# Kernel tuning notes

Hardware: AMD Instinct MI355X
Metric: run time of the kernel (lower is better)

Reference implementation:

```python
import jax, jax.numpy as jnp
import numpy as np


def conv2d(x, w, stride=1, padding=0):
    # x: [N,Ci,H,W], w: [Co,Ci,Kh,Kw]
    return jax.lax.conv_general_dilated(
        x, w, window_strides=(stride, stride),
        padding=[(padding, padding), (padding, padding)],
        dimension_numbers=('NCHW', 'OIHW', 'NCHW'))


def adder2d(x, w, stride=1, padding=0):
    """AdderNet L1-distance conv: out[n,co,ho,wo] = -sum_{ci,kh,kw} |x_patch - w[co,ci,kh,kw]|."""
    N, Ci, H, W = x.shape
    Co, _, K, _ = w.shape
    xp = jnp.pad(x, ((0, 0), (0, 0), (padding, padding), (padding, padding)))
    Ho = (H + 2 * padding - K) // stride + 1
    Wo = (W + 2 * padding - K) // stride + 1
    acc = jnp.zeros((N, Co, Ho, Wo), x.dtype)
    for kh in range(K):  # small fixed loop over kernel taps (<=9)
        for kw in range(K):
            xs = xp[:, :, kh:kh + Ho * stride:stride, kw:kw + Wo * stride:stride]  # [N,Ci,Ho,Wo]
            diff = jnp.abs(xs[:, None] - w[None, :, :, kh, kw, None, None])  # [N,Co,Ci,Ho,Wo]
            acc = acc - diff.sum(axis=2)
    return acc


def batchnorm(x, gamma, beta, mean, var, eps=1e-5):
    inv = gamma / jnp.sqrt(var + eps)
    return x * inv[None, :, None, None] + (beta - mean * inv)[None, :, None, None]


def setup_inputs() -> dict:
    key = jax.random.key(0)
    ks = jax.random.split(key, 16)
    N, C, H, W = 4, 128, 28, 28
    inp = {
        'x': jax.random.normal(ks[0], (N, C, H, W), jnp.float32),
        'w_shift1': jax.random.normal(ks[1], (C, C, 1, 1), jnp.float32) * 0.1,
        'w_add1': jax.random.normal(ks[2], (C, C, 1, 1), jnp.float32) * 0.1,
        'bn1_gamma': jax.random.uniform(ks[3], (C,), jnp.float32, 0.5, 1.5),
        'bn1_beta': jax.random.normal(ks[4], (C,), jnp.float32) * 0.1,
        'bn1_mean': jax.random.normal(ks[5], (C,), jnp.float32),
        'bn1_var': jax.random.uniform(ks[6], (C,), jnp.float32, 0.5, 1.5),
        'w_shift2': jax.random.normal(ks[7], (C, C, 3, 3), jnp.float32) * 0.05,
        'w_add2': jax.random.normal(ks[8], (C, C, 3, 3), jnp.float32) * 0.05,
        'bn2_gamma': jax.random.uniform(ks[9], (C,), jnp.float32, 0.5, 1.5),
        'bn2_beta': jax.random.normal(ks[10], (C,), jnp.float32) * 0.1,
        'bn2_mean': jax.random.normal(ks[11], (C,), jnp.float32),
        'bn2_var': jax.random.uniform(ks[12], (C,), jnp.float32, 0.5, 1.5),
    }
    return inp


def reference(x, w_shift1, w_add1, bn1_gamma, bn1_beta, bn1_mean, bn1_var,
              w_shift2, w_add2, bn2_gamma, bn2_beta, bn2_mean, bn2_var):
    identity = x
    # conv1: 1x1 shift conv -> 1x1 adder
    out = conv2d(x, w_shift1, stride=1, padding=0)
    out = adder2d(out, w_add1, stride=1, padding=0)
    out = jax.nn.relu(batchnorm(out, bn1_gamma, bn1_beta, bn1_mean, bn1_var))
    # conv2: 3x3 shift conv (stride=1, pad=1) -> 3x3 adder (stride=1, pad=1)
    out = conv2d(out, w_shift2, stride=1, padding=1)
    out = adder2d(out, w_add2, stride=1, padding=1)
    out = jax.nn.relu(batchnorm(out, bn2_gamma, bn2_beta, bn2_mean, bn2_var))
    return jax.nn.relu(out + identity)
```

## Files before the change

kernel.cpp:

```cpp
#include <hip/hip_runtime.h>
#include <math.h>

constexpr int C   = 128;
constexpr int HW  = 784;
constexpr int PW  = 30;
constexpr int PHW = 900;

#define ABS_ACC(acc, d) asm("v_add_f32 %0, %0, abs(%1)" : "+v"(acc) : "v"(d))

__device__ inline void tile_map2(int wg, int& n, int& h0, int& w0) {
    int region = wg & 7;
    int idx    = wg >> 3;
    n = region >> 1;
    int half = region & 1;
    int th = half * 7 + idx / 14;
    int tw = idx % 14;
    h0 = th * 2;
    w0 = tw * 2;
}

__device__ inline void tile_map4(int wg, int& n, int& h0, int& w0, int& co0) {
    int region = wg & 7;
    int rest   = wg >> 3;
    n = region >> 1;
    int half = region & 1;
    co0 = (rest & 1) * 64;
    int idx = rest >> 1;
    int th = idx / 7, tw = idx % 7;
    h0 = half * 14 + th * 2;
    w0 = tw * 4;
}

__device__ inline void zero_border2(float* plane, int h0, int w0) {
    if (h0 == 0) {
        plane[w0 + 1] = 0.f; plane[w0 + 2] = 0.f;
        if (w0 == 0)  plane[0]  = 0.f;
        if (w0 == 26) plane[29] = 0.f;
    }
    if (h0 == 26) {
        plane[29 * PW + w0 + 1] = 0.f; plane[29 * PW + w0 + 2] = 0.f;
        if (w0 == 0)  plane[29 * PW]      = 0.f;
        if (w0 == 26) plane[29 * PW + 29] = 0.f;
    }
    if (w0 == 0)  { plane[(h0 + 1) * PW]      = 0.f; plane[(h0 + 2) * PW]      = 0.f; }
    if (w0 == 26) { plane[(h0 + 1) * PW + 29] = 0.f; plane[(h0 + 2) * PW + 29] = 0.f; }
}

__device__ inline void zero_border4(float* plane, int h0, int w0) {
    if (h0 == 0) {
#pragma unroll
        for (int c = 0; c < 4; ++c) plane[w0 + 1 + c] = 0.f;
        if (w0 == 0)  plane[0]  = 0.f;
        if (w0 == 24) plane[29] = 0.f;
    }
    if (h0 == 26) {
#pragma unroll
        for (int c = 0; c < 4; ++c) plane[29 * PW + w0 + 1 + c] = 0.f;
        if (w0 == 0)  plane[29 * PW]      = 0.f;
        if (w0 == 24) plane[29 * PW + 29] = 0.f;
    }
    if (w0 == 0)  { plane[(h0 + 1) * PW]      = 0.f; plane[(h0 + 2) * PW]      = 0.f; }
    if (w0 == 24) { plane[(h0 + 1) * PW + 29] = 0.f; plane[(h0 + 2) * PW + 29] = 0.f; }
}

__global__ __launch_bounds__(256) void reorder_w(const float* __restrict__ w2,
                                                 const float* __restrict__ a2,
                                                 const float* __restrict__ w1,
                                                 const float* __restrict__ a1,
                                                 float* __restrict__ w2r,
                                                 float* __restrict__ a2r,
                                                 float* __restrict__ w1r,
                                                 float* __restrict__ a1r) {
    int idx = blockIdx.x * 256 + threadIdx.x;
    const int T9 = C * C * 9;
    const int T1 = C * C;
    if (idx < 2 * T9) {
        const float* src = w2; float* dst = w2r;
        if (idx >= T9) { idx -= T9; src = a2; dst = a2r; }
        int co = idx & 127;
        int r  = idx >> 7;
        int k  = r % 9;
        int ci = r / 9;
        dst[idx] = src[(co * C + ci) * 9 + k];
        return;
    }
    idx -= 2 * T9;
    if (idx >= 2 * T1) return;
    const float* src = w1; float* dst = w1r;
    if (idx >= T1) { idx -= T1; src = a1; dst = a1r; }
    int co = idx & 127;
    int ci = idx >> 7;
    dst[idx] = src[co * C + ci];
}

__global__ __launch_bounds__(256, 8) void stage1(const float* __restrict__ x,
                                                 const float* __restrict__ w1r,
                                                 const float* __restrict__ a1r,
                                                 const float* __restrict__ g1,
                                                 const float* __restrict__ b1,
                                                 const float* __restrict__ m1,
                                                 const float* __restrict__ v1,
                                                 float* __restrict__ t1p) {
    __shared__ float Xs[C][4];
    __shared__ float Ys[C][4];
    __shared__ float Rs[C][4];
    int n, h0, w0;
    tile_map2(blockIdx.x, n, h0, w0);
    int t   = threadIdx.x;
    int co  = t & 127;
    int ciq = t >> 7;
    int ci0 = ciq * 64;

#pragma unroll
    for (int e = t; e < 512; e += 256) {
        int ci = e >> 2, p = e & 3, r = p >> 1, c = p & 1;
        Xs[ci][p] = x[(n * C + ci) * HW + (h0 + r) * 28 + w0 + c];
    }
    __syncthreads();

    float4 a = make_float4(0.f, 0.f, 0.f, 0.f);
    const float* wp = w1r + co;
#pragma unroll 4
    for (int i = 0; i < 64; ++i) {
        int ci = ci0 + i;
        float wv = wp[ci * C];
        float4 xv = *reinterpret_cast<const float4*>(&Xs[ci][0]);
        a.x = fmaf(xv.x, wv, a.x);
        a.y = fmaf(xv.y, wv, a.y);
        a.z = fmaf(xv.z, wv, a.z);
        a.w = fmaf(xv.w, wv, a.w);
    }
    if (ciq) *reinterpret_cast<float4*>(&Rs[co][0]) = a;
    __syncthreads();
    if (ciq == 0) {
        float4 r = *reinterpret_cast<const float4*>(&Rs[co][0]);
        a.x += r.x; a.y += r.y; a.z += r.z; a.w += r.w;
        *reinterpret_cast<float4*>(&Ys[co][0]) = a;
    }
    __syncthreads();

    float d0 = 0.f, d1 = 0.f, d2 = 0.f, d3 = 0.f;
    const float* ap = a1r + co;
#pragma unroll 4
    for (int i = 0; i < 64; ++i) {
        int ci = ci0 + i;
        float av = ap[ci * C];
        float4 yv = *reinterpret_cast<const float4*>(&Ys[ci][0]);
        float e0 = yv.x - av; ABS_ACC(d0, e0);
        float e1 = yv.y - av; ABS_ACC(d1, e1);
        float e2 = yv.z - av; ABS_ACC(d2, e2);
        float e3 = yv.w - av; ABS_ACC(d3, e3);
    }
    if (ciq) *reinterpret_cast<float4*>(&Rs[co][0]) = make_float4(d0, d1, d2, d3);
    __syncthreads();
    if (ciq == 0) {
        float4 r = *reinterpret_cast<const float4*>(&Rs[co][0]);
        d0 += r.x; d1 += r.y; d2 += r.z; d3 += r.w;
        float inv = g1[co] / sqrtf(v1[co] + 1e-5f);
        float off = b1[co] - m1[co] * inv;
        float* plane = t1p + (n * C + co) * PHW;
        float* dst = plane + (h0 + 1) * PW + (w0 + 1);
        dst[0]      = fmaxf(-d0 * inv + off, 0.f);
        dst[1]      = fmaxf(-d1 * inv + off, 0.f);
        dst[PW + 0] = fmaxf(-d2 * inv + off, 0.f);
        dst[PW + 1] = fmaxf(-d3 * inv + off, 0.f);
        zero_border2(plane, h0, w0);
    }
}

__global__ __launch_bounds__(256, 8) void conv3x3(const float* __restrict__ t1p,
                                                  const float* __restrict__ w2r,
                                                  float* __restrict__ t2p) {
    __shared__ float Rs[3][64][8];
    int n, h0, w0, co0;
    tile_map4(blockIdx.x, n, h0, w0, co0);
    int t   = threadIdx.x;
    int col = t & 63;
    int co  = co0 + col;
    int ciq = t >> 6;
    int ci0u = __builtin_amdgcn_readfirstlane(ciq * 32);

    const float* sp0 = t1p + n * C * PHW + h0 * PW + w0;
    const float* wb  = w2r + co;
    float acc[2][4] = {{0.f,0.f,0.f,0.f},{0.f,0.f,0.f,0.f}};

#pragma unroll 2
    for (int i = 0; i < 32; ++i) {
        int ci = ci0u + i;
        const float* wp = wb + ci * 9 * C;
        float wk[9];
#pragma unroll
        for (int k = 0; k < 9; ++k) wk[k] = wp[k * C];
        const float* sp = sp0 + ci * PHW;
        float xr[4][6];
#pragma unroll
        for (int r = 0; r < 4; ++r)
#pragma unroll
            for (int c = 0; c < 6; ++c) xr[r][c] = sp[r * PW + c];
#pragma unroll
        for (int kh = 0; kh < 3; ++kh)
#pragma unroll
            for (int kw = 0; kw < 3; ++kw) {
                float wv = wk[kh * 3 + kw];
#pragma unroll
                for (int pr = 0; pr < 2; ++pr)
#pragma unroll
                    for (int pc = 0; pc < 4; ++pc)
                        acc[pr][pc] = fmaf(xr[pr + kh][pc + kw], wv, acc[pr][pc]);
            }
    }
    if (ciq) {
        *reinterpret_cast<float4*>(&Rs[ciq - 1][col][0]) = make_float4(acc[0][0], acc[0][1], acc[0][2], acc[0][3]);
        *reinterpret_cast<float4*>(&Rs[ciq - 1][col][4]) = make_float4(acc[1][0], acc[1][1], acc[1][2], acc[1][3]);
    }
    __syncthreads();
    if (ciq == 0) {
#pragma unroll
        for (int q = 0; q < 3; ++q) {
            float4 r0 = *reinterpret_cast<const float4*>(&Rs[q][col][0]);
            float4 r1 = *reinterpret_cast<const float4*>(&Rs[q][col][4]);
            acc[0][0] += r0.x; acc[0][1] += r0.y; acc[0][2] += r0.z; acc[0][3] += r0.w;
            acc[1][0] += r1.x; acc[1][1] += r1.y; acc[1][2] += r1.z; acc[1][3] += r1.w;
        }
        float* plane = t2p + (n * C + co) * PHW;
        float* dst = plane + (h0 + 1) * PW + (w0 + 1);
#pragma unroll
        for (int pc = 0; pc < 4; ++pc) dst[pc]      = acc[0][pc];
#pragma unroll
        for (int pc = 0; pc < 4; ++pc) dst[PW + pc] = acc[1][pc];
        zero_border4(plane, h0, w0);
    }
}

__global__ __launch_bounds__(256, 8) void adder3x3(const float* __restrict__ t2p,
                                                   const float* __restrict__ a2r,
                                                   const float* __restrict__ x0,
                                                   const float* __restrict__ g2,
                                                   const float* __restrict__ b2,
                                                   const float* __restrict__ m2,
                                                   const float* __restrict__ v2,
                                                   float* __restrict__ out) {
    __shared__ float Rs[3][64][8];
    int n, h0, w0, co0;
    tile_map4(blockIdx.x, n, h0, w0, co0);
    int t   = threadIdx.x;
    int col = t & 63;
    int co  = co0 + col;
    int ciq = t >> 6;
    int ci0u = __builtin_amdgcn_readfirstlane(ciq * 32);

    const float* sp0 = t2p + n * C * PHW + h0 * PW + w0;
    const float* ab  = a2r + co;
    float acc[2][4] = {{0.f,0.f,0.f,0.f},{0.f,0.f,0.f,0.f}};

#pragma unroll 2
    for (int i = 0; i < 32; ++i) {
        int ci = ci0u + i;
        const float* wp = ab + ci * 9 * C;
        float wk[9];
#pragma unroll
        for (int k = 0; k < 9; ++k) wk[k] = wp[k * C];
        const float* sp = sp0 + ci * PHW;
        float xr[4][6];
#pragma unroll
        for (int r = 0; r < 4; ++r)
#pragma unroll
            for (int c = 0; c < 6; ++c) xr[r][c] = sp[r * PW + c];
#pragma unroll
        for (int kh = 0; kh < 3; ++kh)
#pragma unroll
            for (int kw = 0; kw < 3; ++kw) {
                float wv = wk[kh * 3 + kw];
#pragma unroll
                for (int pr = 0; pr < 2; ++pr)
#pragma unroll
                    for (int pc = 0; pc < 4; ++pc) {
                        float e = xr[pr + kh][pc + kw] - wv;
                        ABS_ACC(acc[pr][pc], e);
                    }
            }
    }
    if (ciq) {
        *reinterpret_cast<float4*>(&Rs[ciq - 1][col][0]) = make_float4(acc[0][0], acc[0][1], acc[0][2], acc[0][3]);
        *reinterpret_cast<float4*>(&Rs[ciq - 1][col][4]) = make_float4(acc[1][0], acc[1][1], acc[1][2], acc[1][3]);
    }
    __syncthreads();
    if (ciq == 0) {
#pragma unroll
        for (int q = 0; q < 3; ++q) {
            float4 r0 = *reinterpret_cast<const float4*>(&Rs[q][col][0]);
            float4 r1 = *reinterpret_cast<const float4*>(&Rs[q][col][4]);
            acc[0][0] += r0.x; acc[0][1] += r0.y; acc[0][2] += r0.z; acc[0][3] += r0.w;
            acc[1][0] += r1.x; acc[1][1] += r1.y; acc[1][2] += r1.z; acc[1][3] += r1.w;
        }
        float inv = g2[co] / sqrtf(v2[co] + 1e-5f);
        float off = b2[co] - m2[co] * inv;
        int base = (n * C + co) * HW + h0 * 28 + w0;
#pragma unroll
        for (int pr = 0; pr < 2; ++pr) {
#pragma unroll
            for (int pc = 0; pc < 4; ++pc) {
                float z = fmaxf(-acc[pr][pc] * inv + off, 0.f);
                z += x0[base + pr * 28 + pc];
                out[base + pr * 28 + pc] = fmaxf(z, 0.f);
            }
        }
    }
}

extern "C" void kernel_launch(void* const* d_in, const int* in_sizes, int n_in,
                              void* d_out, int out_size, void* d_ws, size_t ws_size,
                              hipStream_t stream) {
    const float* x   = (const float*)d_in[0];
    const float* w1  = (const float*)d_in[1];
    const float* a1  = (const float*)d_in[2];
    const float* g1  = (const float*)d_in[3];
    const float* b1  = (const float*)d_in[4];
    const float* m1  = (const float*)d_in[5];
    const float* v1  = (const float*)d_in[6];
    const float* w2  = (const float*)d_in[7];
    const float* a2  = (const float*)d_in[8];
    const float* g2  = (const float*)d_in[9];
    const float* b2  = (const float*)d_in[10];
    const float* m2  = (const float*)d_in[11];
    const float* v2  = (const float*)d_in[12];
    float* out = (float*)d_out;

    float* ws  = (float*)d_ws;
    float* t1p = ws;
    float* t2p = t1p + 4 * C * PHW;
    float* w2r = t2p + 4 * C * PHW;
    float* a2r = w2r + C * C * 9;
    float* w1r = a2r + C * C * 9;
    float* a1r = w1r + C * C;

    const int reorder_total = 2 * C * C * 9 + 2 * C * C;
    reorder_w<<<(reorder_total + 255) / 256, 256, 0, stream>>>(w2, a2, w1, a1, w2r, a2r, w1r, a1r);
    stage1<<<784, 256, 0, stream>>>(x, w1r, a1r, g1, b1, m1, v1, t1p);
    conv3x3<<<784, 256, 0, stream>>>(t1p, w2r, t2p);
    adder3x3<<<784, 256, 0, stream>>>(t2p, a2r, x, g2, b2, m2, v2, out);
}
```

Before: 69.37 us.

## Enlarge 3x3 conv/adder tiles to 4x4 outputs with 8-way channel split

The 3x3 conv and adder kernels now compute 4x4 output tiles per thread instead of 2x4. Blocks grow to 512 threads, with the input channels split eight ways and reduced through a larger shared buffer. The padded plane row pitch goes from 30 to 32 floats for better-aligned row access. The larger tiles increase reuse of loaded input rows and weights, at the cost of more registers per thread, half as many blocks, and a longer shared-memory reduction.

Result: slower. 73.16 us (+5.5%).

```diff
diff --git a/kernel.cpp b/kernel.cpp
--- a/kernel.cpp
+++ b/kernel.cpp
@@ -3,8 +3,9 @@
 
 constexpr int C   = 128;
 constexpr int HW  = 784;
-constexpr int PW  = 30;
-constexpr int PHW = 900;
+constexpr int PW  = 32;
+constexpr int PH  = 30;
+constexpr int PHW = PW * PH;
 
 #define ABS_ACC(acc, d) asm("v_add_f32 %0, %0, abs(%1)" : "+v"(acc) : "v"(d))
 
@@ -19,15 +20,13 @@
     w0 = tw * 2;
 }
 
-__device__ inline void tile_map4(int wg, int& n, int& h0, int& w0, int& co0) {
+__device__ inline void tile_map44(int wg, int& n, int& h0, int& w0, int& co0) {
     int region = wg & 7;
-    int rest   = wg >> 3;
-    n = region >> 1;
-    int half = region & 1;
-    co0 = (rest & 1) * 64;
-    int idx = rest >> 1;
+    int idx    = wg >> 3;
+    n   = region >> 1;
+    co0 = (region & 1) * 64;
     int th = idx / 7, tw = idx % 7;
-    h0 = half * 14 + th * 2;
+    h0 = th * 4;
     w0 = tw * 4;
 }
 
@@ -46,21 +45,27 @@
     if (w0 == 26) { plane[(h0 + 1) * PW + 29] = 0.f; plane[(h0 + 2) * PW + 29] = 0.f; }
 }
 
-__device__ inline void zero_border4(float* plane, int h0, int w0) {
+__device__ inline void zero_border44(float* plane, int h0, int w0) {
     if (h0 == 0) {
 #pragma unroll
         for (int c = 0; c < 4; ++c) plane[w0 + 1 + c] = 0.f;
         if (w0 == 0)  plane[0]  = 0.f;
         if (w0 == 24) plane[29] = 0.f;
     }
-    if (h0 == 26) {
+    if (h0 == 24) {
 #pragma unroll
         for (int c = 0; c < 4; ++c) plane[29 * PW + w0 + 1 + c] = 0.f;
         if (w0 == 0)  plane[29 * PW]      = 0.f;
         if (w0 == 24) plane[29 * PW + 29] = 0.f;
     }
-    if (w0 == 0)  { plane[(h0 + 1) * PW]      = 0.f; plane[(h0 + 2) * PW]      = 0.f; }
-    if (w0 == 24) { plane[(h0 + 1) * PW + 29] = 0.f; plane[(h0 + 2) * PW + 29] = 0.f; }
+    if (w0 == 0) {
+#pragma unroll
+        for (int r = 0; r < 4; ++r) plane[(h0 + 1 + r) * PW] = 0.f;
+    }
+    if (w0 == 24) {
+#pragma unroll
+        for (int r = 0; r < 4; ++r) plane[(h0 + 1 + r) * PW + 29] = 0.f;
+    }
 }
 
 __global__ __launch_bounds__(256) void reorder_w(const float* __restrict__ w2,
@@ -168,33 +173,35 @@
     }
 }
 
-__global__ __launch_bounds__(256, 8) void conv3x3(const float* __restrict__ t1p,
+__global__ __launch_bounds__(512, 8) void conv3x3(const float* __restrict__ t1p,
                                                   const float* __restrict__ w2r,
                                                   float* __restrict__ t2p) {
-    __shared__ float Rs[3][64][8];
+    __shared__ float Rs[7][64][16];
     int n, h0, w0, co0;
-    tile_map4(blockIdx.x, n, h0, w0, co0);
+    tile_map44(blockIdx.x, n, h0, w0, co0);
     int t   = threadIdx.x;
     int col = t & 63;
     int co  = co0 + col;
     int ciq = t >> 6;
-    int ci0u = __builtin_amdgcn_readfirstlane(ciq * 32);
+    int ci0u = __builtin_amdgcn_readfirstlane(ciq * 16);
 
     const float* sp0 = t1p + n * C * PHW + h0 * PW + w0;
     const float* wb  = w2r + co;
-    float acc[2][4] = {{0.f,0.f,0.f,0.f},{0.f,0.f,0.f,0.f}};
+    float acc[16];
+#pragma unroll
+    for (int j = 0; j < 16; ++j) acc[j] = 0.f;
 
 #pragma unroll 2
-    for (int i = 0; i < 32; ++i) {
+    for (int i = 0; i < 16; ++i) {
         int ci = ci0u + i;
         const float* wp = wb + ci * 9 * C;
         float wk[9];
 #pragma unroll
         for (int k = 0; k < 9; ++k) wk[k] = wp[k * C];
         const float* sp = sp0 + ci * PHW;
-        float xr[4][6];
-#pragma unroll
-        for (int r = 0; r < 4; ++r)
+        float xr[6][6];
+#pragma unroll
+        for (int r = 0; r < 6; ++r)
 #pragma unroll
             for (int c = 0; c < 6; ++c) xr[r][c] = sp[r * PW + c];
 #pragma unroll
@@ -203,36 +210,35 @@
             for (int kw = 0; kw < 3; ++kw) {
                 float wv = wk[kh * 3 + kw];
 #pragma unroll
-                for (int pr = 0; pr < 2; ++pr)
+                for (int pr = 0; pr < 4; ++pr)
 #pragma unroll
                     for (int pc = 0; pc < 4; ++pc)
-                        acc[pr][pc] = fmaf(xr[pr + kh][pc + kw], wv, acc[pr][pc]);
+                        acc[pr * 4 + pc] = fmaf(xr[pr + kh][pc + kw], wv, acc[pr * 4 + pc]);
             }
     }
     if (ciq) {
-        *reinterpret_cast<float4*>(&Rs[ciq - 1][col][0]) = make_float4(acc[0][0], acc[0][1], acc[0][2], acc[0][3]);
-        *reinterpret_cast<float4*>(&Rs[ciq - 1][col][4]) = make_float4(acc[1][0], acc[1][1], acc[1][2], acc[1][3]);
+#pragma unroll
+        for (int j = 0; j < 4; ++j)
+            *reinterpret_cast<float4*>(&Rs[ciq - 1][col][j * 4]) =
+                make_float4(acc[j * 4], acc[j * 4 + 1], acc[j * 4 + 2], acc[j * 4 + 3]);
     }
     __syncthreads();
     if (ciq == 0) {
 #pragma unroll
-        for (int q = 0; q < 3; ++q) {
-            float4 r0 = *reinterpret_cast<const float4*>(&Rs[q][col][0]);
-            float4 r1 = *reinterpret_cast<const float4*>(&Rs[q][col][4]);
-            acc[0][0] += r0.x; acc[0][1] += r0.y; acc[0][2] += r0.z; acc[0][3] += r0.w;
-            acc[1][0] += r1.x; acc[1][1] += r1.y; acc[1][2] += r1.z; acc[1][3] += r1.w;
-        }
+        for (int q = 0; q < 7; ++q)
+#pragma unroll
+            for (int j = 0; j < 16; ++j) acc[j] += Rs[q][col][j];
         float* plane = t2p + (n * C + co) * PHW;
         float* dst = plane + (h0 + 1) * PW + (w0 + 1);
 #pragma unroll
-        for (int pc = 0; pc < 4; ++pc) dst[pc]      = acc[0][pc];
-#pragma unroll
-        for (int pc = 0; pc < 4; ++pc) dst[PW + pc] = acc[1][pc];
-        zero_border4(plane, h0, w0);
-    }
-}
-
-__global__ __launch_bounds__(256, 8) void adder3x3(const float* __restrict__ t2p,
+        for (int pr = 0; pr < 4; ++pr)
+#pragma unroll
+            for (int pc = 0; pc < 4; ++pc) dst[pr * PW + pc] = acc[pr * 4 + pc];
+        zero_border44(plane, h0, w0);
+    }
+}
+
+__global__ __launch_bounds__(512, 8) void adder3x3(const float* __restrict__ t2p,
                                                    const float* __restrict__ a2r,
                                                    const float* __restrict__ x0,
                                                    const float* __restrict__ g2,
@@ -240,30 +246,32 @@
                                                    const float* __restrict__ m2,
                                                    const float* __restrict__ v2,
                                                    float* __restrict__ out) {
-    __shared__ float Rs[3][64][8];
+    __shared__ float Rs[7][64][16];
     int n, h0, w0, co0;
-    tile_map4(blockIdx.x, n, h0, w0, co0);
+    tile_map44(blockIdx.x, n, h0, w0, co0);
     int t   = threadIdx.x;
     int col = t & 63;
     int co  = co0 + col;
     int ciq = t >> 6;
-    int ci0u = __builtin_amdgcn_readfirstlane(ciq * 32);
+    int ci0u = __builtin_amdgcn_readfirstlane(ciq * 16);
 
     const float* sp0 = t2p + n * C * PHW + h0 * PW + w0;
     const float* ab  = a2r + co;
-    float acc[2][4] = {{0.f,0.f,0.f,0.f},{0.f,0.f,0.f,0.f}};
+    float acc[16];
+#pragma unroll
+    for (int j = 0; j < 16; ++j) acc[j] = 0.f;
 
 #pragma unroll 2
-    for (int i = 0; i < 32; ++i) {
+    for (int i = 0; i < 16; ++i) {
         int ci = ci0u + i;
         const float* wp = ab + ci * 9 * C;
         float wk[9];
 #pragma unroll
         for (int k = 0; k < 9; ++k) wk[k] = wp[k * C];
         const float* sp = sp0 + ci * PHW;
-        float xr[4][6];
-#pragma unroll
-        for (int r = 0; r < 4; ++r)
+        float xr[6][6];
+#pragma unroll
+        for (int r = 0; r < 6; ++r)
 #pragma unroll
             for (int c = 0; c < 6; ++c) xr[r][c] = sp[r * PW + c];
 #pragma unroll
@@ -272,39 +280,37 @@
             for (int kw = 0; kw < 3; ++kw) {
                 float wv = wk[kh * 3 + kw];
 #pragma unroll
-                for (int pr = 0; pr < 2; ++pr)
+                for (int pr = 0; pr < 4; ++pr)
 #pragma unroll
                     for (int pc = 0; pc < 4; ++pc) {
                         float e = xr[pr + kh][pc + kw] - wv;
-                        ABS_ACC(acc[pr][pc], e);
+                        ABS_ACC(acc[pr * 4 + pc], e);
                     }
             }
     }
     if (ciq) {
-        *reinterpret_cast<float4*>(&Rs[ciq - 1][col][0]) = make_float4(acc[0][0], acc[0][1], acc[0][2], acc[0][3]);
-        *reinterpret_cast<float4*>(&Rs[ciq - 1][col][4]) = make_float4(acc[1][0], acc[1][1], acc[1][2], acc[1][3]);
+#pragma unroll
+        for (int j = 0; j < 4; ++j)
+            *reinterpret_cast<float4*>(&Rs[ciq - 1][col][j * 4]) =
+                make_float4(acc[j * 4], acc[j * 4 + 1], acc[j * 4 + 2], acc[j * 4 + 3]);
     }
     __syncthreads();
     if (ciq == 0) {
 #pragma unroll
-        for (int q = 0; q < 3; ++q) {
-            float4 r0 = *reinterpret_cast<const float4*>(&Rs[q][col][0]);
-            float4 r1 = *reinterpret_cast<const float4*>(&Rs[q][col][4]);
-            acc[0][0] += r0.x; acc[0][1] += r0.y; acc[0][2] += r0.z; acc[0][3] += r0.w;
-            acc[1][0] += r1.x; acc[1][1] += r1.y; acc[1][2] += r1.z; acc[1][3] += r1.w;
-        }
+        for (int q = 0; q < 7; ++q)
+#pragma unroll
+            for (int j = 0; j < 16; ++j) acc[j] += Rs[q][col][j];
         float inv = g2[co] / sqrtf(v2[co] + 1e-5f);
         float off = b2[co] - m2[co] * inv;
         int base = (n * C + co) * HW + h0 * 28 + w0;
 #pragma unroll
-        for (int pr = 0; pr < 2; ++pr) {
+        for (int pr = 0; pr < 4; ++pr)
 #pragma unroll
             for (int pc = 0; pc < 4; ++pc) {
-                float z = fmaxf(-acc[pr][pc] * inv + off, 0.f);
+                float z = fmaxf(-acc[pr * 4 + pc] * inv + off, 0.f);
                 z += x0[base + pr * 28 + pc];
                 out[base + pr * 28 + pc] = fmaxf(z, 0.f);
             }
-        }
     }
 }
 
@@ -337,6 +343,6 @@
     const int reorder_total = 2 * C * C * 9 + 2 * C * C;
     reorder_w<<<(reorder_total + 255) / 256, 256, 0, stream>>>(w2, a2, w1, a1, w2r, a2r, w1r, a1r);
     stage1<<<784, 256, 0, stream>>>(x, w1r, a1r, g1, b1, m1, v1, t1p);
-    conv3x3<<<784, 256, 0, stream>>>(t1p, w2r, t2p);
-    adder3x3<<<784, 256, 0, stream>>>(t2p, a2r, x, g2, b2, m2, v2, out);
-}
+    conv3x3<<<392, 512, 0, stream>>>(t1p, w2r, t2p);
+    adder3x3<<<392, 512, 0, stream>>>(t2p, a2r, x, g2, b2, m2, v2, out);
+}
```

## Pad plane rows to 32 and software-pipeline 3x3 conv/adder loads with vector loads

Applied to the files above, without the earlier changes.

Widens the padded intermediate plane pitch from 30 to 32 floats so each thread's input rows are 16-byte aligned and can be fetched with float4+float2 loads instead of scalar loads. The 3x3 conv and adder main loops become explicitly double-buffered, prefetching the next channel's weights and inputs while computing the current one. Launch bounds drop from 8 to 4 waves per SIMD to make room for the extra registers, trading occupancy for latency hiding. The padded layout also uses more memory, and the last iteration issues a redundant wrap-around prefetch.

Result: no change. 69.85 us (+0.7%).

```diff
diff --git a/kernel.cpp b/kernel.cpp
--- a/kernel.cpp
+++ b/kernel.cpp
@@ -3,8 +3,9 @@
 
 constexpr int C   = 128;
 constexpr int HW  = 784;
-constexpr int PW  = 30;
-constexpr int PHW = 900;
+constexpr int PW  = 32;
+constexpr int PH  = 30;
+constexpr int PHW = PW * PH;
 
 #define ABS_ACC(acc, d) asm("v_add_f32 %0, %0, abs(%1)" : "+v"(acc) : "v"(d))
 
@@ -61,6 +62,66 @@
     }
     if (w0 == 0)  { plane[(h0 + 1) * PW]      = 0.f; plane[(h0 + 2) * PW]      = 0.f; }
     if (w0 == 24) { plane[(h0 + 1) * PW + 29] = 0.f; plane[(h0 + 2) * PW + 29] = 0.f; }
+}
+
+__device__ __forceinline__ void loadw9(const float* __restrict__ wb, int ci, float wk[9]) {
+    const float* wp = wb + ci * 9 * C;
+#pragma unroll
+    for (int k = 0; k < 9; ++k) wk[k] = wp[k * C];
+}
+
+__device__ __forceinline__ void loadx46(const float* __restrict__ sp0, int ci,
+                                        float4 rr[4], float2 ss[4]) {
+    const float* sp = sp0 + ci * PHW;
+#pragma unroll
+    for (int r = 0; r < 4; ++r) {
+        rr[r] = *reinterpret_cast<const float4*>(sp + r * PW);
+        ss[r] = *reinterpret_cast<const float2*>(sp + r * PW + 4);
+    }
+}
+
+__device__ __forceinline__ void body_conv(const float wk[9], const float4 rr[4],
+                                          const float2 ss[4], float acc[2][4]) {
+    float xr[4][6];
+#pragma unroll
+    for (int r = 0; r < 4; ++r) {
+        xr[r][0] = rr[r].x; xr[r][1] = rr[r].y; xr[r][2] = rr[r].z;
+        xr[r][3] = rr[r].w; xr[r][4] = ss[r].x; xr[r][5] = ss[r].y;
+    }
+#pragma unroll
+    for (int kh = 0; kh < 3; ++kh)
+#pragma unroll
+        for (int kw = 0; kw < 3; ++kw) {
+            float wv = wk[kh * 3 + kw];
+#pragma unroll
+            for (int pr = 0; pr < 2; ++pr)
+#pragma unroll
+                for (int pc = 0; pc < 4; ++pc)
+                    acc[pr][pc] = fmaf(xr[pr + kh][pc + kw], wv, acc[pr][pc]);
+        }
+}
+
+__device__ __forceinline__ void body_adder(const float wk[9], const float4 rr[4],
+                                           const float2 ss[4], float acc[2][4]) {
+    float xr[4][6];
+#pragma unroll
+    for (int r = 0; r < 4; ++r) {
+        xr[r][0] = rr[r].x; xr[r][1] = rr[r].y; xr[r][2] = rr[r].z;
+        xr[r][3] = rr[r].w; xr[r][4] = ss[r].x; xr[r][5] = ss[r].y;
+    }
+#pragma unroll
+    for (int kh = 0; kh < 3; ++kh)
+#pragma unroll
+        for (int kw = 0; kw < 3; ++kw) {
+            float wv = wk[kh * 3 + kw];
+#pragma unroll
+            for (int pr = 0; pr < 2; ++pr)
+#pragma unroll
+                for (int pc = 0; pc < 4; ++pc) {
+                    float e = xr[pr + kh][pc + kw] - wv;
+                    ABS_ACC(acc[pr][pc], e);
+                }
+        }
 }
 
 __global__ __launch_bounds__(256) void reorder_w(const float* __restrict__ w2,
@@ -168,7 +229,7 @@
     }
 }
 
-__global__ __launch_bounds__(256, 8) void conv3x3(const float* __restrict__ t1p,
+__global__ __launch_bounds__(256, 4) void conv3x3(const float* __restrict__ t1p,
                                                   const float* __restrict__ w2r,
                                                   float* __restrict__ t2p) {
     __shared__ float Rs[3][64][8];
@@ -184,31 +245,24 @@
     const float* wb  = w2r + co;
     float acc[2][4] = {{0.f,0.f,0.f,0.f},{0.f,0.f,0.f,0.f}};
 
-#pragma unroll 2
-    for (int i = 0; i < 32; ++i) {
-        int ci = ci0u + i;
-        const float* wp = wb + ci * 9 * C;
-        float wk[9];
-#pragma unroll
-        for (int k = 0; k < 9; ++k) wk[k] = wp[k * C];
-        const float* sp = sp0 + ci * PHW;
-        float xr[4][6];
-#pragma unroll
-        for (int r = 0; r < 4; ++r)
-#pragma unroll
-            for (int c = 0; c < 6; ++c) xr[r][c] = sp[r * PW + c];
-#pragma unroll
-        for (int kh = 0; kh < 3; ++kh)
-#pragma unroll
-            for (int kw = 0; kw < 3; ++kw) {
-                float wv = wk[kh * 3 + kw];
-#pragma unroll
-                for (int pr = 0; pr < 2; ++pr)
-#pragma unroll
-                    for (int pc = 0; pc < 4; ++pc)
-                        acc[pr][pc] = fmaf(xr[pr + kh][pc + kw], wv, acc[pr][pc]);
-            }
-    }
+    float  wkA[9], wkB[9];
+    float4 rA[4], rB[4];
+    float2 sA[4], sB[4];
+
+    loadw9(wb, ci0u, wkA);
+    loadx46(sp0, ci0u, rA, sA);
+#pragma unroll 1
+    for (int i = 0; i < 32; i += 2) {
+        int ciB = ci0u + i + 1;
+        loadw9(wb, ciB, wkB);
+        loadx46(sp0, ciB, rB, sB);
+        body_conv(wkA, rA, sA, acc);
+        int ciA = ci0u + ((i + 2) & 31);
+        loadw9(wb, ciA, wkA);
+        loadx46(sp0, ciA, rA, sA);
+        body_conv(wkB, rB, sB, acc);
+    }
+
     if (ciq) {
         *reinterpret_cast<float4*>(&Rs[ciq - 1][col][0]) = make_float4(acc[0][0], acc[0][1], acc[0][2], acc[0][3]);
         *reinterpret_cast<float4*>(&Rs[ciq - 1][col][4]) = make_float4(acc[1][0], acc[1][1], acc[1][2], acc[1][3]);
@@ -232,7 +286,7 @@
     }
 }
 
-__global__ __launch_bounds__(256, 8) void adder3x3(const float* __restrict__ t2p,
+__global__ __launch_bounds__(256, 4) void adder3x3(const float* __restrict__ t2p,
                                                    const float* __restrict__ a2r,
                                                    const float* __restrict__ x0,
                                                    const float* __restrict__ g2,
@@ -250,36 +304,27 @@
     int ci0u = __builtin_amdgcn_readfirstlane(ciq * 32);
 
     const float* sp0 = t2p + n * C * PHW + h0 * PW + w0;
-    const float* ab  = a2r + co;
+    const float* wb  = a2r + co;
     float acc[2][4] = {{0.f,0.f,0.f,0.f},{0.f,0.f,0.f,0.f}};
 
-#pragma unroll 2
-    for (int i = 0; i < 32; ++i) {
-        int ci = ci0u + i;
-        const float* wp = ab + ci * 9 * C;
-        float wk[9];
-#pragma unroll
-        for (int k = 0; k < 9; ++k) wk[k] = wp[k * C];
-        const float* sp = sp0 + ci * PHW;
-        float xr[4][6];
-#pragma unroll
-        for (int r = 0; r < 4; ++r)
-#pragma unroll
-            for (int c = 0; c < 6; ++c) xr[r][c] = sp[r * PW + c];
-#pragma unroll
-        for (int kh = 0; kh < 3; ++kh)
-#pragma unroll
-            for (int kw = 0; kw < 3; ++kw) {
-                float wv = wk[kh * 3 + kw];
-#pragma unroll
-                for (int pr = 0; pr < 2; ++pr)
-#pragma unroll
-                    for (int pc = 0; pc < 4; ++pc) {
-                        float e = xr[pr + kh][pc + kw] - wv;
-                        ABS_ACC(acc[pr][pc], e);
-                    }
-            }
-    }
+    float  wkA[9], wkB[9];
+    float4 rA[4], rB[4];
+    float2 sA[4], sB[4];
+
+    loadw9(wb, ci0u, wkA);
+    loadx46(sp0, ci0u, rA, sA);
+#pragma unroll 1
+    for (int i = 0; i < 32; i += 2) {
+        int ciB = ci0u + i + 1;
+        loadw9(wb, ciB, wkB);
+        loadx46(sp0, ciB, rB, sB);
+        body_adder(wkA, rA, sA, acc);
+        int ciA = ci0u + ((i + 2) & 31);
+        loadw9(wb, ciA, wkA);
+        loadx46(sp0, ciA, rA, sA);
+        body_adder(wkB, rB, sB, acc);
+    }
+
     if (ciq) {
         *reinterpret_cast<float4*>(&Rs[ciq - 1][col][0]) = make_float4(acc[0][0], acc[0][1], acc[0][2], acc[0][3]);
         *reinterpret_cast<float4*>(&Rs[ciq - 1][col][4]) = make_float4(acc[1][0], acc[1][1], acc[1][2], acc[1][3]);
```

## Stage 3x3 input patches in LDS with padded 32-wide planes for vector loads

Applied to the files above, without the earlier changes.

Pads the intermediate planes to a row pitch of 32 floats so rows are 16-byte aligned. In both 3x3 kernels, the block cooperatively loads the 4x8 input patch for all 128 channels into LDS with float4 global loads, then each thread reads its 4x6 window with float4+float2 LDS loads. The aim is to replace many scalar, uniform-address global loads per channel with shared vectorized staging. The cost is an extra barrier, 16KB of LDS per block that may reduce occupancy, and a larger intermediate buffer footprint.

Measured after the change: 68.16 us. Within noise of the previous version (-1.7%).

```diff
diff --git a/kernel.cpp b/kernel.cpp
--- a/kernel.cpp
+++ b/kernel.cpp
@@ -3,8 +3,9 @@
 
 constexpr int C   = 128;
 constexpr int HW  = 784;
-constexpr int PW  = 30;
-constexpr int PHW = 900;
+constexpr int PW  = 32;
+constexpr int PH  = 30;
+constexpr int PHW = PW * PH;
 
 #define ABS_ACC(acc, d) asm("v_add_f32 %0, %0, abs(%1)" : "+v"(acc) : "v"(d))
 
@@ -171,6 +172,7 @@
 __global__ __launch_bounds__(256, 8) void conv3x3(const float* __restrict__ t1p,
                                                   const float* __restrict__ w2r,
                                                   float* __restrict__ t2p) {
+    __shared__ float Xl[C][4][8];
     __shared__ float Rs[3][64][8];
     int n, h0, w0, co0;
     tile_map4(blockIdx.x, n, h0, w0, co0);
@@ -178,25 +180,35 @@
     int col = t & 63;
     int co  = co0 + col;
     int ciq = t >> 6;
-    int ci0u = __builtin_amdgcn_readfirstlane(ciq * 32);
+    int ci0 = ciq * 32;
 
     const float* sp0 = t1p + n * C * PHW + h0 * PW + w0;
-    const float* wb  = w2r + co;
+#pragma unroll
+    for (int e = t; e < 1024; e += 256) {
+        int ci = e >> 3, rh = e & 7, r = rh >> 1, half = rh & 1;
+        *reinterpret_cast<float4*>(&Xl[ci][r][half * 4]) =
+            *reinterpret_cast<const float4*>(sp0 + ci * PHW + r * PW + half * 4);
+    }
+    __syncthreads();
+
+    const float* wb = w2r + co;
     float acc[2][4] = {{0.f,0.f,0.f,0.f},{0.f,0.f,0.f,0.f}};
 
 #pragma unroll 2
     for (int i = 0; i < 32; ++i) {
-        int ci = ci0u + i;
+        int ci = ci0 + i;
         const float* wp = wb + ci * 9 * C;
         float wk[9];
 #pragma unroll
         for (int k = 0; k < 9; ++k) wk[k] = wp[k * C];
-        const float* sp = sp0 + ci * PHW;
         float xr[4][6];
 #pragma unroll
-        for (int r = 0; r < 4; ++r)
-#pragma unroll
-            for (int c = 0; c < 6; ++c) xr[r][c] = sp[r * PW + c];
+        for (int r = 0; r < 4; ++r) {
+            float4 q = *reinterpret_cast<const float4*>(&Xl[ci][r][0]);
+            float2 s = *reinterpret_cast<const float2*>(&Xl[ci][r][4]);
+            xr[r][0] = q.x; xr[r][1] = q.y; xr[r][2] = q.z;
+            xr[r][3] = q.w; xr[r][4] = s.x; xr[r][5] = s.y;
+        }
 #pragma unroll
         for (int kh = 0; kh < 3; ++kh)
 #pragma unroll
@@ -209,6 +221,7 @@
                         acc[pr][pc] = fmaf(xr[pr + kh][pc + kw], wv, acc[pr][pc]);
             }
     }
+
     if (ciq) {
         *reinterpret_cast<float4*>(&Rs[ciq - 1][col][0]) = make_float4(acc[0][0], acc[0][1], acc[0][2], acc[0][3]);
         *reinterpret_cast<float4*>(&Rs[ciq - 1][col][4]) = make_float4(acc[1][0], acc[1][1], acc[1][2], acc[1][3]);
@@ -240,6 +253,7 @@
                                                    const float* __restrict__ m2,
                                                    const float* __restrict__ v2,
                                                    float* __restrict__ out) {
+    __shared__ float Xl[C][4][8];
     __shared__ float Rs[3][64][8];
     int n, h0, w0, co0;
     tile_map4(blockIdx.x, n, h0, w0, co0);
@@ -247,25 +261,35 @@
     int col = t & 63;
     int co  = co0 + col;
     int ciq = t >> 6;
-    int ci0u = __builtin_amdgcn_readfirstlane(ciq * 32);
+    int ci0 = ciq * 32;
 
     const float* sp0 = t2p + n * C * PHW + h0 * PW + w0;
-    const float* ab  = a2r + co;
+#pragma unroll
+    for (int e = t; e < 1024; e += 256) {
+        int ci = e >> 3, rh = e & 7, r = rh >> 1, half = rh & 1;
+        *reinterpret_cast<float4*>(&Xl[ci][r][half * 4]) =
+            *reinterpret_cast<const float4*>(sp0 + ci * PHW + r * PW + half * 4);
+    }
+    __syncthreads();
+
+    const float* ab = a2r + co;
     float acc[2][4] = {{0.f,0.f,0.f,0.f},{0.f,0.f,0.f,0.f}};
 
 #pragma unroll 2
     for (int i = 0; i < 32; ++i) {
-        int ci = ci0u + i;
+        int ci = ci0 + i;
         const float* wp = ab + ci * 9 * C;
         float wk[9];
 #pragma unroll
         for (int k = 0; k < 9; ++k) wk[k] = wp[k * C];
-        const float* sp = sp0 + ci * PHW;
         float xr[4][6];
 #pragma unroll
-        for (int r = 0; r < 4; ++r)
-#pragma unroll
-            for (int c = 0; c < 6; ++c) xr[r][c] = sp[r * PW + c];
+        for (int r = 0; r < 4; ++r) {
+            float4 q = *reinterpret_cast<const float4*>(&Xl[ci][r][0]);
+            float2 s = *reinterpret_cast<const float2*>(&Xl[ci][r][4]);
+            xr[r][0] = q.x; xr[r][1] = q.y; xr[r][2] = q.z;
+            xr[r][3] = q.w; xr[r][4] = s.x; xr[r][5] = s.y;
+        }
 #pragma unroll
         for (int kh = 0; kh < 3; ++kh)
 #pragma unroll
@@ -280,6 +304,7 @@
                     }
             }
     }
+
     if (ciq) {
         *reinterpret_cast<float4*>(&Rs[ciq - 1][col][0]) = make_float4(acc[0][0], acc[0][1], acc[0][2], acc[0][3]);
         *reinterpret_cast<float4*>(&Rs[ciq - 1][col][4]) = make_float4(acc[1][0], acc[1][1], acc[1][2], acc[1][3]);
```
